# Optimization experiments

Hardware: AMD Instinct MI355X
Metric: run time of the kernel (lower is better)

Reference implementation:

```python
import jax, jax.numpy as jnp
import numpy as np

REPLACE_PROB = 0.1  # init kwarg replace_prob


def _log_trans():
    """Build log P(x_t | x_{t-2}, x_{t-1}) exactly as the torch module does.

    torch: tmp[i][j] = [p, s, p]; tmp[2][1] = [0, s/(p+s), p/(p+s)]
           cond2d[j][i] = Categorical(tmp[i][j]), sampled as
           cond2d[x_{t-2}][x_{t-1}]  =>  probs = tmp[x_{t-1}][x_{t-2}]
    """
    p = REPLACE_PROB
    s = 1.0 - 2.0 * p
    tmp = np.tile(np.array([p, s, p], dtype=np.float32), (3, 3, 1))  # (3,3,3)
    tmp[2, 1] = np.array([0.0, s / (p + s), p / (p + s)], dtype=np.float32)
    table = np.transpose(tmp, (1, 0, 2))  # table[prev2, prev1, :] = tmp[prev1, prev2, :]
    return jnp.log(jnp.asarray(table))  # -inf for the disallowed entry is fine


def _gen_mask(key, n_batch, n_win):
    """2nd-order Markov chain over alphabet {0,1,2}, vectorized over batch.
    Returns gather indices of shape (n_batch, n_win) with values in [0, n_win-1].
    """
    logT = _log_trans()  # (3,3,3)
    init = (jnp.ones(n_batch, jnp.int32), jnp.ones(n_batch, jnp.int32))  # mindex[:,0:2]=1
    keys = jax.random.split(key, n_win - 2)

    def step(carry, k):
        p2, p1 = carry
        s = jax.random.categorical(k, logT[p2, p1]).astype(jnp.int32)  # (B,)
        return (p1, s), s

    _, samples = jax.lax.scan(step, init, keys)  # (n_win-2, B)
    ones = jnp.ones((n_batch, 1), jnp.int32)
    # original: mindex has n_win+1 cols, cols [0,1]=1, col n_win=1, then drops col 0
    m = jnp.concatenate([ones, samples.T, ones], axis=1)  # (B, n_win)
    return m + jnp.arange(n_win, dtype=jnp.int32) - 1


def setup_inputs() -> dict:
    key = jax.random.key(0)
    x = jax.random.normal(key, (32, 512, 4096), dtype=jnp.float32)  # (B, I, T)
    return {"x": x}


def reference(x):
    n_batch, _, n_win = x.shape
    mindex = _gen_mask(jax.random.key(42), n_batch, n_win)  # (B, T)
    # per-batch index_select along the time axis
    return jax.vmap(lambda xb, mb: xb[:, mb])(x, mindex)
```

## Files before the change

### kernel.cpp

```cpp
#include <hip/hip_runtime.h>
#include <cmath>
#include <cstdint>

#define NB 32
#define NI 512
#define NT 4096
#define NSTEPS (NT - 2)
#define THR 512
#define SPT 8
#define GBLK 4096
#define GITER 16

__device__ __forceinline__ uint32_t rotl32(uint32_t v, unsigned d) {
  return (v << d) | (v >> (32u - d));
}

__device__ __forceinline__ void threefry2x32(uint32_t k0, uint32_t k1,
                                             uint32_t& x0, uint32_t& x1) {
  const uint32_t k2 = k0 ^ k1 ^ 0x1BD11BDAu;
  x0 += k0; x1 += k1;
#define TF_R(rot) { x0 += x1; x1 = rotl32(x1, rot); x1 ^= x0; }
  TF_R(13) TF_R(15) TF_R(26) TF_R(6)
  x0 += k1; x1 += k2 + 1u;
  TF_R(17) TF_R(29) TF_R(16) TF_R(24)
  x0 += k2; x1 += k0 + 2u;
  TF_R(13) TF_R(15) TF_R(26) TF_R(6)
  x0 += k0; x1 += k1 + 3u;
  TF_R(17) TF_R(29) TF_R(16) TF_R(24)
  x0 += k1; x1 += k2 + 4u;
  TF_R(13) TF_R(15) TF_R(26) TF_R(6)
  x0 += k2; x1 += k0 + 5u;
#undef TF_R
}

__device__ __forceinline__ float gumbel_from_bits(uint32_t bits) {
  uint32_t fb = (bits >> 9) | 0x3F800000u;
  float f = __uint_as_float(fb) - 1.0f;
  float u = fmaxf(f, __FLT_MIN__);
  float lg = (float)log((double)u);
  return -(float)log((double)(-lg));
}

__device__ __forceinline__ uint32_t comp_map(uint32_t a, uint32_t b) {
  uint32_t r = 0;
#pragma unroll
  for (int st = 0; st < 4; ++st) {
    uint32_t as = (a >> (2 * st)) & 3u;
    uint32_t bs = (b >> (2 * as)) & 3u;
    r |= bs << (2 * st);
  }
  return r;
}

__global__ void k_sab(uint32_t* __restrict__ sab32,
                      float LP, float LS, float LB1, float LB2) {
  int t = blockIdx.x * blockDim.x + threadIdx.x;
  int b = blockIdx.y;
  if (t >= NSTEPS) return;
  uint32_t k0 = 0u, k1 = (uint32_t)t;
  threefry2x32(0u, 42u, k0, k1);
  float g[3];
#pragma unroll
  for (int j = 0; j < 3; ++j) {
    uint32_t x0 = 0u, x1 = (uint32_t)(3 * b + j);
    threefry2x32(k0, k1, x0, x1);
    g[j] = gumbel_from_bits(x0 ^ x1);
  }
  float vA0 = LP + g[0], vA1 = LS + g[1], vA2 = LP + g[2];
  int sA = 0; float m = vA0;
  if (vA1 > m) { m = vA1; sA = 1; }
  if (vA2 > m) { sA = 2; }
  int sB = (LB2 + g[2] > LB1 + g[1]) ? 2 : 1;
  uint32_t v = (uint32_t)(sA | (sB << 4));
  __hip_atomic_store(&sab32[(size_t)b * NT + t], v,
                     __ATOMIC_RELAXED, __HIP_MEMORY_SCOPE_AGENT);
}

__global__ void __launch_bounds__(THR) k_scan(uint32_t* __restrict__ sab32,
                                              uint32_t* __restrict__ mword) {
  const int b = blockIdx.x;
  const int tid = threadIdx.x;

  __shared__ uint32_t smap[THR];
  __shared__ uint8_t lds_m[NT];

  uint32_t packA = 0, packB = 0;
  const uint32_t* src = sab32 + (size_t)b * NT;
#pragma unroll
  for (int k = 0; k < SPT; ++k) {
    int t = tid * SPT + k;
    if (t >= NSTEPS) break;
    uint32_t w = __hip_atomic_load(&src[t], __ATOMIC_RELAXED,
                                   __HIP_MEMORY_SCOPE_AGENT);
    packA |= (w & 0xFu) << (4 * k);
    packB |= ((w >> 4) & 0xFu) << (4 * k);
  }

  uint32_t cmap;
  {
    uint32_t st0 = 0, st1 = 1, st2 = 2, st3 = 3;
#pragma unroll
    for (int k = 0; k < SPT; ++k) {
      int t = tid * SPT + k;
      if (t >= NSTEPS) break;
      uint32_t sA = (packA >> (4 * k)) & 0xFu;
      uint32_t sB = (packB >> (4 * k)) & 0xFu;
#define STEP(st) { uint32_t s = (st == 3u) ? sB : sA; st = (st == 1u && s == 2u) ? 3u : s; }
      STEP(st0) STEP(st1) STEP(st2) STEP(st3)
#undef STEP
    }
    cmap = st0 | (st1 << 2) | (st2 << 4) | (st3 << 6);
  }
  smap[tid] = cmap;
  __syncthreads();
  for (int d = 1; d < THR; d <<= 1) {
    uint32_t prev = (tid >= d) ? smap[tid - d] : 0u;
    __syncthreads();
    if (tid >= d) smap[tid] = comp_map(prev, smap[tid]);
    __syncthreads();
  }
  uint32_t st = (tid == 0) ? 1u : ((smap[tid - 1] >> 2) & 3u);

#pragma unroll
  for (int k = 0; k < SPT; ++k) {
    int t = tid * SPT + k;
    if (t >= NSTEPS) break;
    uint32_t sA = (packA >> (4 * k)) & 0xFu;
    uint32_t sB = (packB >> (4 * k)) & 0xFu;
    uint32_t s = (st == 3u) ? sB : sA;
    st = (st == 1u && s == 2u) ? 3u : s;
    lds_m[t + 1] = (uint8_t)s;
  }
  if (tid == 0) lds_m[0] = 1;
  if (tid == THR - 1) lds_m[NT - 1] = 1;
  __syncthreads();

  const uint32_t* wsrc = (const uint32_t*)lds_m;
  uint32_t* dst = mword + (size_t)b * (NT / 4);
#pragma unroll
  for (int r = 0; r < (NT / 4) / THR; ++r) {
    int w = r * THR + tid;
    __hip_atomic_store(&dst[w], wsrc[w],
                       __ATOMIC_RELAXED, __HIP_MEMORY_SCOPE_AGENT);
  }
}

__global__ void __launch_bounds__(256) k_gather(const float* __restrict__ x,
                                                uint32_t* __restrict__ mword,
                                                float* __restrict__ out) {
  const int q0  = blockIdx.x * 256 + threadIdx.x;
  const int b0  = q0 >> 19;
  const int rem = q0 & ((1 << 19) - 1);
  const int i   = rem >> 10;
  const int w   = rem & 1023;
  const int t   = w << 2;

  const size_t mbase = ((size_t)b0 << 10) | (uint32_t)w;
  const size_t rowstep = ((size_t)2 * NI) << 12;
  size_t row = ((size_t)b0 * NI + i) << 12;

  uint32_t mw = __hip_atomic_load(&mword[mbase], __ATOMIC_RELAXED,
                                  __HIP_MEMORY_SCOPE_AGENT);
#pragma unroll 1
  for (int k = 0; k < GITER; ++k) {
    uint32_t mw_next = 0u;
    if (k + 1 < GITER) {
      mw_next = __hip_atomic_load(&mword[mbase + ((size_t)(2 * (k + 1)) << 10)],
                                  __ATOMIC_RELAXED, __HIP_MEMORY_SCOPE_AGENT);
    }
    const float* xb = x + row;
    float4 o;
    o.x = xb[(int)( mw        & 0xFFu) + t + 0 - 1];
    o.y = xb[(int)((mw >>  8) & 0xFFu) + t + 1 - 1];
    o.z = xb[(int)((mw >> 16) & 0xFFu) + t + 2 - 1];
    o.w = xb[(int)((mw >> 24) & 0xFFu) + t + 3 - 1];
    *(float4*)(out + row + t) = o;
    mw = mw_next;
    row += rowstep;
  }
}

extern "C" void kernel_launch(void* const* d_in, const int* in_sizes, int n_in,
                              void* d_out, int out_size, void* d_ws, size_t ws_size,
                              hipStream_t stream) {
  const float* x = (const float*)d_in[0];
  float* out = (float*)d_out;

  uint8_t* ws = (uint8_t*)d_ws;
  uint32_t* sab32 = (uint32_t*)ws;
  uint32_t* mword = (uint32_t*)(ws + 524288);

  const double pd = 0.1, sd = 1.0 - 2.0 * 0.1;
  const float pf = (float)pd, sf = (float)sd;
  const float b1 = (float)(sd / (pd + sd));
  const float b2 = (float)(pd / (pd + sd));
  const float LP  = (float)log((double)pf);
  const float LS  = (float)log((double)sf);
  const float LB1 = (float)log((double)b1);
  const float LB2 = (float)log((double)b2);

  dim3 g1((NSTEPS + 255) / 256, NB);
  k_sab<<<g1, 256, 0, stream>>>(sab32, LP, LS, LB1, LB2);
  k_scan<<<NB, THR, 0, stream>>>(sab32, mword);
  k_gather<<<GBLK, 256, 0, stream>>>(x, mword, out);
}
```

Measured before the change: 120.5 us.

## Gather via vector loads and wave shuffles, eight outputs per thread

```diff
diff --git a/kernel.cpp b/kernel.cpp
--- a/kernel.cpp
+++ b/kernel.cpp
@@ -8,7 +8,7 @@
 #define NSTEPS (NT - 2)
 #define THR 512
 #define SPT 8
-#define GBLK 4096
+#define GBLK 2048
 #define GITER 16
 
 __device__ __forceinline__ uint32_t rotl32(uint32_t v, unsigned d) {
@@ -148,33 +148,67 @@
 __global__ void __launch_bounds__(256) k_gather(const float* __restrict__ x,
                                                 uint32_t* __restrict__ mword,
                                                 float* __restrict__ out) {
-  const int q0  = blockIdx.x * 256 + threadIdx.x;
-  const int b0  = q0 >> 19;
-  const int rem = q0 & ((1 << 19) - 1);
-  const int i   = rem >> 10;
-  const int w   = rem & 1023;
-  const int t   = w << 2;
-
-  const size_t mbase = ((size_t)b0 << 10) | (uint32_t)w;
+  const int tid = threadIdx.x;
+  const int q0  = blockIdx.x * 256 + tid;
+  const int b0  = q0 >> 18;
+  const int rem = q0 & ((1 << 18) - 1);
+  const int i   = rem >> 9;
+  const int wp  = rem & 511;
+  const int t   = wp << 3;
+  const int lane = tid & 63;
+
+  const size_t mbase = ((size_t)b0 << 10) | (uint32_t)(wp << 1);
   const size_t rowstep = ((size_t)2 * NI) << 12;
   size_t row = ((size_t)b0 * NI + i) << 12;
 
-  uint32_t mw = __hip_atomic_load(&mword[mbase], __ATOMIC_RELAXED,
-                                  __HIP_MEMORY_SCOPE_AGENT);
+  const bool ld_lo = (lane == 0)  && (wp > 0);
+  const bool ld_hi = (lane == 63) && (wp < 511);
+
+  uint64_t mw = __hip_atomic_load((const uint64_t*)&mword[mbase],
+                                  __ATOMIC_RELAXED, __HIP_MEMORY_SCOPE_AGENT);
 #pragma unroll 1
   for (int k = 0; k < GITER; ++k) {
-    uint32_t mw_next = 0u;
+    uint64_t mw_next = 0ull;
     if (k + 1 < GITER) {
-      mw_next = __hip_atomic_load(&mword[mbase + ((size_t)(2 * (k + 1)) << 10)],
-                                  __ATOMIC_RELAXED, __HIP_MEMORY_SCOPE_AGENT);
+      mw_next = __hip_atomic_load(
+          (const uint64_t*)&mword[mbase + ((size_t)(2 * (k + 1)) << 10)],
+          __ATOMIC_RELAXED, __HIP_MEMORY_SCOPE_AGENT);
     }
     const float* xb = x + row;
-    float4 o;
-    o.x = xb[(int)( mw        & 0xFFu) + t + 0 - 1];
-    o.y = xb[(int)((mw >>  8) & 0xFFu) + t + 1 - 1];
-    o.z = xb[(int)((mw >> 16) & 0xFFu) + t + 2 - 1];
-    o.w = xb[(int)((mw >> 24) & 0xFFu) + t + 3 - 1];
-    *(float4*)(out + row + t) = o;
+    const float4 qa = *(const float4*)(xb + t);
+    const float4 qb = *(const float4*)(xb + t + 4);
+
+    float edge_lo = 0.0f, edge_hi = 0.0f;
+    if (ld_lo) edge_lo = xb[t - 1];
+    if (ld_hi) edge_hi = xb[t + 8];
+
+    float prev = __shfl_up(qb.w, 1);
+    if (lane == 0) prev = edge_lo;
+    float next = __shfl_down(qa.x, 1);
+    if (lane == 63) next = edge_hi;
+
+    const uint32_t m0 = (uint32_t)(mw      ) & 0xFFu;
+    const uint32_t m1 = (uint32_t)(mw >>  8) & 0xFFu;
+    const uint32_t m2 = (uint32_t)(mw >> 16) & 0xFFu;
+    const uint32_t m3 = (uint32_t)(mw >> 24) & 0xFFu;
+    const uint32_t m4 = (uint32_t)(mw >> 32) & 0xFFu;
+    const uint32_t m5 = (uint32_t)(mw >> 40) & 0xFFu;
+    const uint32_t m6 = (uint32_t)(mw >> 48) & 0xFFu;
+    const uint32_t m7 = (uint32_t)(mw >> 56) & 0xFFu;
+
+    float4 oa, ob;
+    oa.x = (m0 == 0u) ? prev : ((m0 == 1u) ? qa.x : qa.y);
+    oa.y = (m1 == 0u) ? qa.x : ((m1 == 1u) ? qa.y : qa.z);
+    oa.z = (m2 == 0u) ? qa.y : ((m2 == 1u) ? qa.z : qa.w);
+    oa.w = (m3 == 0u) ? qa.z : ((m3 == 1u) ? qa.w : qb.x);
+    ob.x = (m4 == 0u) ? qa.w : ((m4 == 1u) ? qb.x : qb.y);
+    ob.y = (m5 == 0u) ? qb.x : ((m5 == 1u) ? qb.y : qb.z);
+    ob.z = (m6 == 0u) ? qb.y : ((m6 == 1u) ? qb.z : qb.w);
+    ob.w = (m7 == 0u) ? qb.z : ((m7 == 1u) ? qb.w : next);
+
+    *(float4*)(out + row + t)     = oa;
+    *(float4*)(out + row + t + 4) = ob;
+
     mw = mw_next;
     row += rowstep;
   }
```

After: 127.1 us. 1.06x slower.
